# Optimization experiments

Measured on AMD Instinct MI355X. Metric: run time of the kernel, lower is better.

Reference implementation:

```python
import jax, jax.numpy as jnp
import numpy as np
import math

N, E, MUL = 10000, 160000, 128
D = MUL * 4  # 128x0e (128) + 128x1o (384) = 512
NEURONS = 32
EDGE_ATTR_DIM = 32
WEIGHT_NUMEL = 4 * MUL  # 4 uvu tensor-product paths, 128 weights each


def ssp(x):
    return jax.nn.softplus(x) - math.log(2.0)


def irrep_linear(x, W0, b0, W1):
    # o3.Linear on 128x0e+128x1o: mixes mul channels within each irrep, fan-in normalized,
    # bias only on scalar (0e) block.
    s = x[:, :MUL] @ (W0 / jnp.sqrt(MUL)) + b0
    v = x[:, MUL:].reshape(-1, MUL, 3)
    v = jnp.einsum('num,uv->nvm', v, W1) / jnp.sqrt(MUL)
    return jnp.concatenate([s, v.reshape(-1, MUL * 3)], axis=-1)


def inner_product(a, b):
    # InnerProduct: uuu channel-wise irrep inner product, 1/sqrt(dim) normalized
    s = a[:, :MUL] * b[:, :MUL]
    va = a[:, MUL:].reshape(-1, MUL, 3)
    vb = b[:, MUL:].reshape(-1, MUL, 3)
    v = jnp.einsum('num,num->nu', va, vb) / jnp.sqrt(3.0)
    return jnp.concatenate([s, v], axis=-1)


def norm_gate(x, W1, b1, W2, b2):
    # NormGate: per-channel norms of l>0 irreps -> MLP gates -> gate l>0 channels
    v = x[:, MUL:].reshape(-1, MUL, 3)
    norm_v = jnp.sqrt(jnp.sum(v * v, axis=-1) + 1e-12)      # [n, 128]
    f0 = jnp.concatenate([x[:, :MUL], norm_v], axis=-1)     # [n, 256]
    g = jax.nn.silu(f0 @ W1 + b1) @ W2 + b2                 # [n, 256]
    gated = v * g[:, MUL:, None]
    return jnp.concatenate([g[:, :MUL], gated.reshape(-1, MUL * 3)], axis=-1)


def mlp2(x, Wa, Wb):
    # e3nn FullyConnectedNet: fan-in normalized, ssp nonlinearity on hidden layer only
    return ssp(x @ (Wa / jnp.sqrt(Wa.shape[0]))) @ (Wb / jnp.sqrt(Wb.shape[0]))


def setup_inputs():
    key = jax.random.key(0)
    ks = jax.random.split(key, 20)
    r = lambda i, shp: jax.random.normal(ks[i], shp, dtype=jnp.float32)
    return {
        'x': r(0, (N, D)),
        'edge_index': jax.random.randint(ks[1], (2, E), 0, N, dtype=jnp.int32),
        'edge_attr': jax.random.uniform(ks[2], (E, EDGE_ATTR_DIM), dtype=jnp.float32),
        'edge_sh': r(3, (E, 4)),
        'Wp0': r(4, (MUL, MUL)), 'bp0': jnp.zeros((MUL,), jnp.float32), 'Wp1': r(5, (MUL, MUL)),
        'ngW1': r(6, (2 * MUL, 2 * MUL)) / 16.0, 'ngb1': jnp.zeros((2 * MUL,), jnp.float32),
        'ngW2': r(7, (2 * MUL, 2 * MUL)) / 16.0, 'ngb2': jnp.zeros((2 * MUL,), jnp.float32),
        'Wn0': r(8, (MUL, MUL)), 'bn0': jnp.zeros((MUL,), jnp.float32), 'Wn1': r(9, (MUL, MUL)),
        'fcnW1': r(10, (EDGE_ATTR_DIM, NEURONS)), 'fcnW2': r(11, (NEURONS, WEIGHT_NUMEL)),
        'l0W1': r(12, (3 * MUL, NEURONS)), 'l0W2': r(13, (NEURONS, WEIGHT_NUMEL)),
        'Wo0': r(14, (MUL, MUL)), 'bo0': jnp.zeros((MUL,), jnp.float32), 'Wo1': r(15, (MUL, MUL)),
    }


def reference(x, edge_index, edge_attr, edge_sh, Wp0, bp0, Wp1, ngW1, ngb1, ngW2, ngb2,
              Wn0, bn0, Wn1, fcnW1, fcnW2, l0W1, l0W2, Wo0, bo0, Wo1):
    edge_dst, edge_src = edge_index[0], edge_index[1]
    # invariant edge descriptor s0 from pre-linear + inner product
    pre_x = irrep_linear(x, Wp0, bp0, Wp1)
    ip = inner_product(pre_x[edge_dst], pre_x[edge_src])[:, MUL:]             # [E,128]
    s0 = jnp.concatenate([pre_x[edge_dst][:, :MUL], pre_x[edge_src][:, :MUL], ip], axis=-1)  # [E,384]
    # norm-gate + linear on node features
    x = norm_gate(x, ngW1, ngb1, ngW2, ngb2)
    x = irrep_linear(x, Wn0, bn0, Wn1)
    self_x = x
    # per-edge tensor-product weights: fc_node(edge_attr) * layer_l0(s0)
    w = mlp2(edge_attr, fcnW1, fcnW2) * mlp2(s0, l0W1, l0W2)                   # [E,512]
    w1, w2, w3, w4 = w[:, :MUL], w[:, MUL:2 * MUL], w[:, 2 * MUL:3 * MUL], w[:, 3 * MUL:]
    xs = x[edge_src]
    xs0 = xs[:, :MUL]                     # [E,128]
    xs1 = xs[:, MUL:].reshape(E, MUL, 3)  # [E,128,3]
    sh0 = edge_sh[:, 0:1]
    sh1 = edge_sh[:, 1:4]
    # uvu CG tensor product paths: 0ex0e->0e, 0ex1o->1o, 1ox0e->1o, 1ox1o->0e
    c0, c1 = 0.5, jnp.sqrt(3.0) / 2.0  # path norm sqrt(ir_out.dim / n_paths)
    out0 = c0 * (w1 * xs0 * sh0 + w4 * jnp.einsum('eum,em->eu', xs1, sh1) / jnp.sqrt(3.0))
    out1 = c1 * (w2[:, :, None] * xs0[:, :, None] * sh1[:, None, :]
                 + w3[:, :, None] * xs1 * sh0[:, :, None])
    edge_feat = jnp.concatenate([out0, out1.reshape(E, MUL * 3)], axis=-1)     # [E,512]
    # scatter-aggregate to destination nodes, residual, output linear
    out = jax.ops.segment_sum(edge_feat, edge_dst, num_segments=N)
    out = out + self_x
    return irrep_linear(out, Wo0, bo0, Wo1)
```

## Files before the change

kernel.cpp:

```cpp
#include <hip/hip_runtime.h>
#include <hip/hip_fp16.h>
#include <math.h>

#define NN 10000
#define EE 160000
#define DPB 8

#define RS128 0.08838834764831845f
#define RS384 0.05103103630798287f
#define RS32  0.17677669529663687f
#define R3    0.57735026918962576f
#define C1V   0.86602540378443865f

typedef _Float16 half8 __attribute__((ext_vector_type(8)));
typedef _Float16 half4 __attribute__((ext_vector_type(4)));
typedef float f32x4 __attribute__((ext_vector_type(4)));

__device__ __forceinline__ float sspf(float x) {
    return fmaxf(x, 0.0f) + log1pf(__expf(-fabsf(x))) - 0.69314718055994530942f;
}

__device__ __forceinline__ void packone(const float* __restrict__ W,
                                        _Float16* __restrict__ P,
                                        int K, int N, int off) {
    const int KS = K >> 5;
    int j = off & 7, lane = (off >> 3) & 63, rest = off >> 9;
    int ks = rest % KS, ct = rest / KS;
    int k = ks * 32 + ((lane >> 4) << 3) + j;
    int c = ct * 16 + (lane & 15);
    P[off] = (_Float16)W[k * N + c];
}

__global__ __launch_bounds__(256) void k_packall(
    const float* __restrict__ Wp0, const float* __restrict__ Wp1,
    const float* __restrict__ Wn0, const float* __restrict__ Wn1,
    const float* __restrict__ Wo0, const float* __restrict__ Wo1,
    const float* __restrict__ ngW1, const float* __restrict__ ngW2,
    const float* __restrict__ l0W1, const float* __restrict__ fcnW1,
    const float* __restrict__ fcnW2, const float* __restrict__ l0W2,
    _Float16* __restrict__ pWp0, _Float16* __restrict__ pWp1,
    _Float16* __restrict__ pWn0, _Float16* __restrict__ pWn1,
    _Float16* __restrict__ pWo0, _Float16* __restrict__ pWo1,
    _Float16* __restrict__ png1, _Float16* __restrict__ png2,
    _Float16* __restrict__ pWc, _Float16* __restrict__ pWa,
    _Float16* __restrict__ Wf_t, _Float16* __restrict__ Wl_t,
    _Float16* __restrict__ pWab, int* __restrict__ degz) {
    int idx = blockIdx.x * 256 + threadIdx.x;
    if (idx < 98304) {
        int seg = idx >> 14, off = idx & 16383;
        if (seg == 0) packone(Wp0, pWp0, 128, 128, off);
        else if (seg == 1) packone(Wp1, pWp1, 128, 128, off);
        else if (seg == 2) packone(Wn0, pWn0, 128, 128, off);
        else if (seg == 3) packone(Wn1, pWn1, 128, 128, off);
        else if (seg == 4) packone(Wo0, pWo0, 128, 128, off);
        else packone(Wo1, pWo1, 128, 128, off);
    } else if (idx < 229376) {
        int r = idx - 98304;
        if (r < 65536) packone(ngW1, png1, 256, 256, r);
        else packone(ngW2, png2, 256, 256, r - 65536);
    } else if (idx < 233472) {
        packone(l0W1 + 256 * 32, pWc, 128, 32, idx - 229376);
    } else if (idx < 234496) {
        packone(fcnW1, pWa, 32, 32, idx - 233472);
    } else if (idx < 250880) {
        int off = idx - 234496;
        int k = off & 31, c = off >> 5;
        Wf_t[c * 32 + k] = (_Float16)fcnW2[k * 512 + c];
        Wl_t[c * 32 + k] = (_Float16)l0W2[k * 512 + c];
    } else if (idx < 259072) {
        int off = idx - 250880;
        int j = off & 7, lane = (off >> 3) & 63, rest = off >> 9;
        int ks = rest & 3, ct = rest >> 2;
        int k = ks * 32 + ((lane >> 4) << 3) + j;
        int c = ct * 16 + (lane & 15);
        pWab[off] = (_Float16)((c < 32) ? l0W1[k * 32 + c]
                                        : l0W1[(128 + k) * 32 + (c - 32)]);
    } else if (idx < 279072) {
        degz[idx - 259072] = 0;
    }
}

__global__ __launch_bounds__(256) void k_node(
    const float* __restrict__ X,
    const _Float16* __restrict__ pWp0, const float* __restrict__ bp0,
    const _Float16* __restrict__ pWp1, const _Float16* __restrict__ pWab,
    const _Float16* __restrict__ png1, const float* __restrict__ ngb1,
    const _Float16* __restrict__ png2, const float* __restrict__ ngb2,
    const _Float16* __restrict__ pWn0, const float* __restrict__ bn0,
    const _Float16* __restrict__ pWn1,
    _Float16* __restrict__ prexv_h, float* __restrict__ pAB,
    _Float16* __restrict__ selfx_h) {
    __shared__ _Float16 f0h[16][264];
    __shared__ _Float16 t1h[16][264];
    __shared__ _Float16 xvh[3][16][136];
    __shared__ _Float16 pvh[3][16][136];
    const int t = threadIdx.x, lane = t & 63, w = t >> 6;
    const int nb = blockIdx.x * 16;
    const int row16 = lane & 15, kg = lane >> 4;
    const f32x4 zero = {0.0f, 0.0f, 0.0f, 0.0f};

    for (int idx = t; idx < 16 * 128; idx += 256) {
        int n = idx >> 7, c4 = idx & 127;
        const float4 v = *(const float4*)(X + (size_t)(nb + n) * 512 + 4 * c4);
        float vals[4] = {v.x, v.y, v.z, v.w};
        int c = 4 * c4;
#pragma unroll
        for (int j = 0; j < 4; ++j) {
            int cc = c + j;
            if (cc < 128) f0h[n][cc] = (_Float16)vals[j];
            else { int d = cc - 128; xvh[d % 3][n][d / 3] = (_Float16)vals[j]; }
        }
    }
    __syncthreads();
    for (int idx = t; idx < 16 * 128; idx += 256) {
        int n = idx >> 7, u = idx & 127;
        float a = (float)xvh[0][n][u], b = (float)xvh[1][n][u], c = (float)xvh[2][n][u];
        f0h[n][128 + u] = (_Float16)sqrtf(fmaf(a, a, fmaf(b, b, fmaf(c, c, 1e-12f))));
    }
    __syncthreads();
    {
        const _Float16* pW = (w == 0) ? pWp0 : pWp1;
        f32x4 acc[8];
#pragma unroll
        for (int ct = 0; ct < 8; ++ct) acc[ct] = zero;
        for (int ks = 0; ks < 4; ++ks) {
            const half8 a = (w == 0)
                ? *(const half8*)&f0h[row16][ks * 32 + kg * 8]
                : *(const half8*)&xvh[w - 1][row16][ks * 32 + kg * 8];
#pragma unroll
            for (int ct = 0; ct < 8; ++ct) {
                const half8 b = *(const half8*)(pW + (((ct * 4 + ks) * 64 + lane) << 3));
                acc[ct] = __builtin_amdgcn_mfma_f32_16x16x32_f16(a, b, acc[ct], 0, 0, 0);
            }
        }
#pragma unroll
        for (int ct = 0; ct < 8; ++ct) {
            const int col = ct * 16 + row16;
            const float bb = (w == 0) ? bp0[col] : 0.0f;
#pragma unroll
            for (int r = 0; r < 4; ++r) {
                const int n = kg * 4 + r;
                const float val = acc[ct][r] * RS128 + bb;
                if (w == 0) t1h[n][col] = (_Float16)val;
                else pvh[w - 1][n][col] = (_Float16)val;
            }
        }
    }
    __syncthreads();
    {
        f32x4 acc = zero;
#pragma unroll
        for (int ks = 0; ks < 4; ++ks) {
            const half8 a = *(const half8*)&t1h[row16][ks * 32 + kg * 8];
            const half8 b = *(const half8*)(pWab + (((w * 4 + ks) * 64 + lane) << 3));
            acc = __builtin_amdgcn_mfma_f32_16x16x32_f16(a, b, acc, 0, 0, 0);
        }
        const int col = w * 16 + row16;
#pragma unroll
        for (int r = 0; r < 4; ++r)
            pAB[(size_t)(nb + kg * 4 + r) * 64 + col] = acc[r];
    }
    for (int idx = t; idx < 16 * 128; idx += 256) {
        int n = idx >> 7, u = idx & 127;
        half4 pv = {pvh[0][n][u], pvh[1][n][u], pvh[2][n][u], t1h[n][u]};
        *(half4*)(prexv_h + (size_t)(nb + n) * 512 + (u << 2)) = pv;
    }
    __syncthreads();
    {
        f32x4 acc[4];
#pragma unroll
        for (int i = 0; i < 4; ++i) acc[i] = zero;
        for (int ks = 0; ks < 8; ++ks) {
            const half8 a = *(const half8*)&f0h[row16][ks * 32 + kg * 8];
#pragma unroll
            for (int c2 = 0; c2 < 4; ++c2) {
                const int ct = 4 * w + c2;
                const half8 b = *(const half8*)(png1 + (((ct * 8 + ks) * 64 + lane) << 3));
                acc[c2] = __builtin_amdgcn_mfma_f32_16x16x32_f16(a, b, acc[c2], 0, 0, 0);
            }
        }
        __syncthreads();
#pragma unroll
        for (int c2 = 0; c2 < 4; ++c2) {
            const int col = (4 * w + c2) * 16 + row16;
            const float bb = ngb1[col];
#pragma unroll
            for (int r = 0; r < 4; ++r) {
                const float z = acc[c2][r] + bb;
                t1h[kg * 4 + r][col] = (_Float16)(z / (1.0f + __expf(-z)));
            }
        }
    }
    __syncthreads();
    {
        f32x4 acc[4];
#pragma unroll
        for (int i = 0; i < 4; ++i) acc[i] = zero;
        for (int ks = 0; ks < 8; ++ks) {
            const half8 a = *(const half8*)&t1h[row16][ks * 32 + kg * 8];
#pragma unroll
            for (int c2 = 0; c2 < 4; ++c2) {
                const int ct = 4 * w + c2;
                const half8 b = *(const half8*)(png2 + (((ct * 8 + ks) * 64 + lane) << 3));
                acc[c2] = __builtin_amdgcn_mfma_f32_16x16x32_f16(a, b, acc[c2], 0, 0, 0);
            }
        }
        __syncthreads();
#pragma unroll
        for (int c2 = 0; c2 < 4; ++c2) {
            const int col = (4 * w + c2) * 16 + row16;
            const float bb = ngb2[col];
#pragma unroll
            for (int r = 0; r < 4; ++r)
                f0h[kg * 4 + r][col] = (_Float16)(acc[c2][r] + bb);
        }
    }
    __syncthreads();
    for (int idx = t; idx < 16 * 128; idx += 256) {
        int n = idx >> 7, u = idx & 127;
        const _Float16 g = f0h[n][128 + u];
        xvh[0][n][u] = xvh[0][n][u] * g;
        xvh[1][n][u] = xvh[1][n][u] * g;
        xvh[2][n][u] = xvh[2][n][u] * g;
    }
    __syncthreads();
    {
        const _Float16* pw = (w == 0) ? pWn0 : pWn1;
        f32x4 acc[8];
#pragma unroll
        for (int ct = 0; ct < 8; ++ct) acc[ct] = zero;
        for (int ks = 0; ks < 4; ++ks) {
            const half8 a = (w == 0)
                ? *(const half8*)&f0h[row16][ks * 32 + kg * 8]
                : *(const half8*)&xvh[w - 1][row16][ks * 32 + kg * 8];
#pragma unroll
            for (int ct = 0; ct < 8; ++ct) {
                const half8 b = *(const half8*)(pw + (((ct * 4 + ks) * 64 + lane) << 3));
                acc[ct] = __builtin_amdgcn_mfma_f32_16x16x32_f16(a, b, acc[ct], 0, 0, 0);
            }
        }
#pragma unroll
        for (int ct = 0; ct < 8; ++ct) {
            const int col = ct * 16 + row16;
            const float bb = (w == 0) ? bn0[col] : 0.0f;
#pragma unroll
            for (int r = 0; r < 4; ++r) {
                const int n = kg * 4 + r;
                const float val = acc[ct][r] * RS128 + bb;
                if (w == 0) f0h[n][col] = (_Float16)val;
                else xvh[w - 1][n][col] = (_Float16)val;
            }
        }
    }
    __syncthreads();
    for (int idx = t; idx < 16 * 128; idx += 256) {
        int n = idx >> 7, u = idx & 127;
        half4 sx = {f0h[n][u], xvh[0][n][u], xvh[1][n][u], xvh[2][n][u]};
        *(half4*)(selfx_h + (size_t)(nb + n) * 512 + (u << 2)) = sx;
    }
}

__global__ __launch_bounds__(256) void k_deg(const int* __restrict__ ei, int* __restrict__ deg) {
    int e = blockIdx.x * 256 + threadIdx.x;
    if (e < EE) atomicAdd(&deg[ei[e]], 1);
}

__global__ __launch_bounds__(1024) void k_scan(const int* __restrict__ deg, int* __restrict__ row_ptr) {
    __shared__ int part[1024];
    const int t = threadIdx.x;
    const int base = t * 10;
    int loc[10];
    int s = 0;
#pragma unroll
    for (int i = 0; i < 10; ++i) {
        int idx = base + i;
        int d = (idx < NN) ? deg[idx] : 0;
        loc[i] = s;
        s += d;
    }
    part[t] = s;
    __syncthreads();
    for (int off = 1; off < 1024; off <<= 1) {
        int v = (t >= off) ? part[t - off] : 0;
        __syncthreads();
        part[t] += v;
        __syncthreads();
    }
    int excl = (t > 0) ? part[t - 1] : 0;
#pragma unroll
    for (int i = 0; i < 10; ++i) {
        int idx = base + i;
        if (idx <= NN) row_ptr[idx] = excl + loc[i];
    }
}

__global__ __launch_bounds__(256) void k_fill(const int* __restrict__ ei,
                                              const int* __restrict__ row_ptr,
                                              int* __restrict__ cursor,
                                              int* __restrict__ csr_eid) {
    int e = blockIdx.x * 256 + threadIdx.x;
    if (e < EE) {
        int d = ei[e];
        int pos = atomicAdd(&cursor[d], 1);
        csr_eid[row_ptr[d] + pos] = e;
    }
}

__global__ __launch_bounds__(256) void k_hidden_m(
    const _Float16* __restrict__ prexv_h, const float* __restrict__ pAB,
    const int* __restrict__ edge_index, const float* __restrict__ edge_attr,
    const int* __restrict__ csr_eid,
    const _Float16* __restrict__ pWc, const _Float16* __restrict__ pWa,
    __half* __restrict__ hh) {
    const int pb = blockIdx.x * 32;
    const int t = threadIdx.x, lane = t & 63, w = t >> 6;
    __shared__ _Float16 ipl[32][132];
    __shared__ _Float16 eal[32][36];
    __shared__ _Float16 h1o[32][32];
    __shared__ _Float16 hao[32][32];
    __shared__ int dsts[32], srcs[32], eids[32];

    if (t < 32) {
        const int id = csr_eid[pb + t];
        eids[t] = id;
        dsts[t] = edge_index[id];
        srcs[t] = edge_index[EE + id];
    }
    __syncthreads();
    for (int idx = t; idx < 32 * 32; idx += 256) {
        int e = idx >> 5, j = idx & 31;
        eal[e][j] = (_Float16)edge_attr[(size_t)eids[e] * 32 + j];
    }
    for (int idx = t; idx < 32 * 128; idx += 256) {
        int e = idx >> 7, u = idx & 127;
        const half4 pd = *(const half4*)(prexv_h + (size_t)dsts[e] * 512 + (u << 2));
        const half4 ps = *(const half4*)(prexv_h + (size_t)srcs[e] * 512 + (u << 2));
        const float ipv = (float)pd.x * (float)ps.x + (float)pd.y * (float)ps.y +
                          (float)pd.z * (float)ps.z;
        ipl[e][u] = (_Float16)(ipv * R3);
    }
    __syncthreads();

    const int row16 = lane & 15, kg = lane >> 4;
    const int mt = w >> 1, ct = w & 1;
    const int e0 = mt * 16;
    const f32x4 zero = {0.0f, 0.0f, 0.0f, 0.0f};
    const int kc = ct * 16 + row16;

    {
        f32x4 acc = zero;
#pragma unroll
        for (int ks = 0; ks < 4; ++ks) {
            const half8 a = *(const half8*)&ipl[e0 + row16][ks * 32 + kg * 8];
            const half8 b = *(const half8*)(pWc + (((ct * 4 + ks) * 64 + lane) << 3));
            acc = __builtin_amdgcn_mfma_f32_16x16x32_f16(a, b, acc, 0, 0, 0);
        }
#pragma unroll
        for (int r = 0; r < 4; ++r) {
            const int e = e0 + kg * 4 + r;
            const float v = acc[r] + pAB[(size_t)dsts[e] * 64 + kc]
                                   + pAB[(size_t)srcs[e] * 64 + 32 + kc];
            h1o[e][kc] = (_Float16)sspf(v * RS384);
        }
    }
    {
        const half8 a = *(const half8*)&eal[e0 + row16][kg * 8];
        const half8 b = *(const half8*)(pWa + ((ct * 64 + lane) << 3));
        f32x4 acc = __builtin_amdgcn_mfma_f32_16x16x32_f16(a, b, zero, 0, 0, 0);
#pragma unroll
        for (int r = 0; r < 4; ++r) {
            const int e = e0 + kg * 4 + r;
            hao[e][kc] = (_Float16)sspf((float)acc[r] * RS32);
        }
    }
    __syncthreads();
    for (int idx = t; idx < 32 * 32; idx += 256) {
        const int e = idx >> 5, j = idx & 31;
        unsigned vv;
        if (j < 16) {
            __half2 h2 = __halves2half2((__half)h1o[e][2 * j], (__half)h1o[e][2 * j + 1]);
            vv = *(unsigned*)&h2;
        } else {
            const int jj = j - 16;
            __half2 h2 = __halves2half2((__half)hao[e][2 * jj], (__half)hao[e][2 * jj + 1]);
            vv = *(unsigned*)&h2;
        }
        ((unsigned*)hh)[(size_t)(pb + e) * 32 + j] = vv;
    }
}

__global__ __launch_bounds__(512) void k_accum(
    const __half* __restrict__ hh, const _Float16* __restrict__ selfx_h,
    const int* __restrict__ edge_index, const float* __restrict__ edge_sh,
    const int* __restrict__ row_ptr, const int* __restrict__ csr_eid,
    const _Float16* __restrict__ Wf_t, const _Float16* __restrict__ Wl_t,
    const _Float16* __restrict__ pWo0, const float* __restrict__ bo0,
    const _Float16* __restrict__ pWo1,
    float* __restrict__ outacc) {
    const int dst0 = blockIdx.x * DPB;
    const int t = threadIdx.x;
    const int lane = t & 63;
    const int wid = t >> 6;
    const int lcol = lane & 15;
    const int kg = lane >> 4;
    const int u = 16 * wid + lcol;
    const int koff = kg * 8;

    __shared__ __align__(16) _Float16 h1s[2][4][16][8];
    __shared__ __align__(16) _Float16 has[2][4][16][8];
    __shared__ float shl[2][16][4];
    __shared__ int srcs[2][16];
    __shared__ int cbeg[DPB], cne[DPB], cchk[DPB + 1];
    __shared__ __align__(16) _Float16 accP[4][16][136];

    if (t < DPB) {
        const int b = row_ptr[dst0 + t];
        cbeg[t] = b;
        cne[t] = row_ptr[dst0 + t + 1] - b;
    }
    for (int idx = t; idx < 4 * 16 * 136; idx += 512)
        ((_Float16*)accP)[idx] = (_Float16)0;
    __syncthreads();
    if (t == 0) {
        int s = 0;
#pragma unroll
        for (int i = 0; i < DPB; ++i) { cchk[i] = s; s += max(1, (cne[i] + 15) >> 4); }
        cchk[DPB] = s;
    }
    half8 bf[4], bl[4];
#pragma unroll
    for (int q = 0; q < 4; ++q) {
        const int col = q * 128 + u;
        bf[q] = *(const half8*)(Wf_t + col * 32 + koff);
        bl[q] = *(const half8*)(Wl_t + col * 32 + koff);
    }
    __syncthreads();
    const int nc = cchk[DPB];
    const float inv32 = 1.0f / 32.0f;

    float acc0 = 0, acc1 = 0, acc2 = 0, acc3 = 0;

    unsigned rhh = 0;
    int rsrc = 0;
    float4 rsh = {0.0f, 0.0f, 0.0f, 0.0f};

    const int se = t >> 5, sw = t & 31;

    auto issue = [&](int ci) {
        int dd = 0;
        while (dd + 1 < DPB && ci >= cchk[dd + 1]) ++dd;
        const int c0 = (ci - cchk[dd]) << 4;
        const int ce = min(16, cne[dd] - c0);
        const int pos = cbeg[dd] + c0;
        rhh = (se < ce) ? ((const unsigned*)hh)[(size_t)(pos + se) * 32 + sw] : 0u;
        if (t < 16) {
            if (t < ce) {
                const int id = csr_eid[pos + t];
                rsrc = edge_index[EE + id];
                rsh = *(const float4*)(edge_sh + (size_t)id * 4);
            } else {
                rsrc = 0;
                rsh = make_float4(0.0f, 0.0f, 0.0f, 0.0f);
            }
        }
    };

    auto flush = [&](int dd) {
        acc0 += __shfl_xor(acc0, 16, 64); acc0 += __shfl_xor(acc0, 32, 64);
        acc1 += __shfl_xor(acc1, 16, 64); acc1 += __shfl_xor(acc1, 32, 64);
        acc2 += __shfl_xor(acc2, 16, 64); acc2 += __shfl_xor(acc2, 32, 64);
        acc3 += __shfl_xor(acc3, 16, 64); acc3 += __shfl_xor(acc3, 32, 64);
        if (lane < 16) {
            const size_t g = (size_t)(dst0 + dd) * 512;
            const half4 sx = *(const half4*)(selfx_h + g + (u << 2));
            accP[0][dd][u] = (_Float16)(acc0 + (float)sx.x);
            accP[1][dd][u] = (_Float16)(acc1 + (float)sx.y);
            accP[2][dd][u] = (_Float16)(acc2 + (float)sx.z);
            accP[3][dd][u] = (_Float16)(acc3 + (float)sx.w);
        }
        acc0 = acc1 = acc2 = acc3 = 0;
    };

    issue(0);
    int cur = 0, cur_dd = 0;
    for (int ci = 0; ci < nc; ++ci) {
        if (sw < 16) ((unsigned*)h1s[cur])[(sw >> 2) * 64 + se * 4 + (sw & 3)] = rhh;
        else         ((unsigned*)has[cur])[((sw - 16) >> 2) * 64 + se * 4 + ((sw - 16) & 3)] = rhh;
        if (t < 16) {
            srcs[cur][t] = rsrc;
            shl[cur][t][0] = rsh.x; shl[cur][t][1] = rsh.y;
            shl[cur][t][2] = rsh.z; shl[cur][t][3] = rsh.w;
        }
        int dd = 0;
        while (dd + 1 < DPB && ci >= cchk[dd + 1]) ++dd;
        const int c0 = (ci - cchk[dd]) << 4;
        const int ce = min(16, cne[dd] - c0);
        if (ci + 1 < nc) issue(ci + 1);
        __syncthreads();
        if (dd != cur_dd) { flush(cur_dd); cur_dd = dd; }

        const half8 haf = *(const half8*)(&has[cur][kg][lcol][0]);
        const half8 h1f = *(const half8*)(&h1s[cur][kg][lcol][0]);
        const f32x4 zero = {0.0f, 0.0f, 0.0f, 0.0f};
        f32x4 A[4], B[4];
#pragma unroll
        for (int q = 0; q < 4; ++q) {
            A[q] = __builtin_amdgcn_mfma_f32_16x16x32_f16(haf, bf[q], zero, 0, 0, 0);
            B[q] = __builtin_amdgcn_mfma_f32_16x16x32_f16(h1f, bl[q], zero, 0, 0, 0);
        }
#pragma unroll
        for (int r = 0; r < 4; ++r) {
            const int e = kg * 4 + r;
            if (e < ce) {
                const float w1 = A[0][r] * B[0][r] * inv32;
                const float w2 = A[1][r] * B[1][r] * inv32;
                const float w3 = A[2][r] * B[2][r] * inv32;
                const float w4 = A[3][r] * B[3][r] * inv32;
                const int src = srcs[cur][e];
                const float sh0 = shl[cur][e][0], s1x = shl[cur][e][1];
                const float s1y = shl[cur][e][2], s1z = shl[cur][e][3];
                const half4 sx = *(const half4*)(selfx_h + (size_t)src * 512 + (u << 2));
                const float xs0 = (float)sx.x;
                const float xv0 = (float)sx.y;
                const float xv1 = (float)sx.z;
                const float xv2 = (float)sx.w;
                const float dv = xv0 * s1x + xv1 * s1y + xv2 * s1z;
                acc0 += 0.5f * (w1 * xs0 * sh0 + w4 * dv * R3);
                acc1 += C1V * (w2 * xs0 * s1x + w3 * xv0 * sh0);
                acc2 += C1V * (w2 * xs0 * s1y + w3 * xv1 * sh0);
                acc3 += C1V * (w2 * xs0 * s1z + w3 * xv2 * sh0);
            }
        }
        cur ^= 1;
    }
    flush(cur_dd);
    __syncthreads();

    {
        const int m = wid >> 1;
        const int ctg = (wid & 1) * 4;
        const _Float16* pW = (m == 0) ? pWo0 : pWo1;
        const f32x4 zero = {0.0f, 0.0f, 0.0f, 0.0f};
        f32x4 acc[4];
#pragma unroll
        for (int i = 0; i < 4; ++i) acc[i] = zero;
        for (int ks = 0; ks < 4; ++ks) {
            const half8 a = *(const half8*)&accP[m][lcol][ks * 32 + koff];
#pragma unroll
            for (int c2 = 0; c2 < 4; ++c2) {
                const int ct = ctg + c2;
                const half8 b = *(const half8*)(pW + (((ct * 4 + ks) * 64 + lane) << 3));
                acc[c2] = __builtin_amdgcn_mfma_f32_16x16x32_f16(a, b, acc[c2], 0, 0, 0);
            }
        }
#pragma unroll
        for (int c2 = 0; c2 < 4; ++c2) {
            const int col = (ctg + c2) * 16 + lcol;
            const float bb = (m == 0) ? bo0[col] : 0.0f;
#pragma unroll
            for (int r = 0; r < 4; ++r) {
                const int row = kg * 4 + r;
                if (row < DPB) {
                    const size_t g = (size_t)(dst0 + row) * 512;
                    const float val = acc[c2][r] * RS128 + bb;
                    if (m == 0) outacc[g + col] = val;
                    else outacc[g + 128 + 3 * col + (m - 1)] = val;
                }
            }
        }
    }
}

extern "C" void kernel_launch(void* const* d_in, const int* in_sizes, int n_in,
                              void* d_out, int out_size, void* d_ws, size_t ws_size,
                              hipStream_t stream) {
    const float* x = (const float*)d_in[0];
    const int* edge_index = (const int*)d_in[1];
    const float* edge_attr = (const float*)d_in[2];
    const float* edge_sh = (const float*)d_in[3];
    const float* Wp0 = (const float*)d_in[4];
    const float* bp0 = (const float*)d_in[5];
    const float* Wp1 = (const float*)d_in[6];
    const float* ngW1 = (const float*)d_in[7];
    const float* ngb1 = (const float*)d_in[8];
    const float* ngW2 = (const float*)d_in[9];
    const float* ngb2 = (const float*)d_in[10];
    const float* Wn0 = (const float*)d_in[11];
    const float* bn0 = (const float*)d_in[12];
    const float* Wn1 = (const float*)d_in[13];
    const float* fcnW1 = (const float*)d_in[14];
    const float* fcnW2 = (const float*)d_in[15];
    const float* l0W1 = (const float*)d_in[16];
    const float* l0W2 = (const float*)d_in[17];
    const float* Wo0 = (const float*)d_in[18];
    const float* bo0 = (const float*)d_in[19];
    const float* Wo1 = (const float*)d_in[20];

    float* out = (float*)d_out;
    _Float16* prexv_h = (_Float16*)d_out;
    _Float16* selfx_h = (_Float16*)d_ws;
    int* deg = (int*)(selfx_h + (size_t)NN * 512);
    int* cursor = deg + NN;
    int* row_ptr = cursor + NN;
    int* csr_eid = row_ptr + NN + 1;
    float* pAB = (float*)(csr_eid + EE);
    __half* hh = (__half*)(pAB + (size_t)NN * 64);
    _Float16* Wf_t = (_Float16*)(hh + (size_t)EE * 64);
    _Float16* Wl_t = Wf_t + 512 * 32;
    _Float16* pWp0 = Wl_t + 512 * 32;
    _Float16* pWp1 = pWp0 + 128 * 128;
    _Float16* pWn0 = pWp1 + 128 * 128;
    _Float16* pWn1 = pWn0 + 128 * 128;
    _Float16* pWo0 = pWn1 + 128 * 128;
    _Float16* pWo1 = pWo0 + 128 * 128;
    _Float16* png1 = pWo1 + 128 * 128;
    _Float16* png2 = png1 + 256 * 256;
    _Float16* pWc  = png2 + 256 * 256;
    _Float16* pWa  = pWc + 128 * 32;
    _Float16* pWab = pWa + 32 * 32;

    k_packall<<<1091, 256, 0, stream>>>(Wp0, Wp1, Wn0, Wn1, Wo0, Wo1, ngW1, ngW2,
                                        l0W1, fcnW1, fcnW2, l0W2,
                                        pWp0, pWp1, pWn0, pWn1, pWo0, pWo1,
                                        png1, png2, pWc, pWa, Wf_t, Wl_t,
                                        pWab, deg);

    k_node<<<NN / 16, 256, 0, stream>>>(x, pWp0, bp0, pWp1, pWab,
                                        png1, ngb1, png2, ngb2, pWn0, bn0, pWn1,
                                        prexv_h, pAB, selfx_h);
    k_deg<<<EE / 256, 256, 0, stream>>>(edge_index, deg);
    k_scan<<<1, 1024, 0, stream>>>(deg, row_ptr);
    k_fill<<<EE / 256, 256, 0, stream>>>(edge_index, row_ptr, cursor, csr_eid);
    k_hidden_m<<<EE / 32, 256, 0, stream>>>(prexv_h, pAB, edge_index, edge_attr, csr_eid,
                                            pWc, pWa, hh);
    k_accum<<<NN / DPB, 512, 0, stream>>>(hh, selfx_h, edge_index, edge_sh, row_ptr, csr_eid,
                                          Wf_t, Wl_t, pWo0, bo0, pWo1, out);
}
```

Measured before the change: 254.4 us.

## Pre-sort src and fp16 edge_sh into CSR order and prefetch gathered source features

k_fill now also writes the source index and a half-precision copy of edge_sh in CSR order, so k_accum no longer follows csr_eid to edge_index and edge_sh. k_accum prefetches the next chunk's gathered selfx rows into registers after the current chunk's compute, overlapping the gather latency with the MFMA work. The Wl_t fragments are reloaded inside the loop instead of being held in registers, which lowers register pressure. The cost is extra global traffic for the reload, fp16 rounding of edge_sh, and a few more workspace writes in k_fill.

```diff
diff --git a/kernel.cpp b/kernel.cpp
--- a/kernel.cpp
+++ b/kernel.cpp
@@ -295,14 +295,22 @@
 }
 
 __global__ __launch_bounds__(256) void k_fill(const int* __restrict__ ei,
+                                              const float* __restrict__ edge_sh,
                                               const int* __restrict__ row_ptr,
                                               int* __restrict__ cursor,
-                                              int* __restrict__ csr_eid) {
+                                              int* __restrict__ csr_eid,
+                                              int* __restrict__ csr_src,
+                                              _Float16* __restrict__ csr_sh) {
     int e = blockIdx.x * 256 + threadIdx.x;
     if (e < EE) {
         int d = ei[e];
-        int pos = atomicAdd(&cursor[d], 1);
-        csr_eid[row_ptr[d] + pos] = e;
+        int s = ei[EE + e];
+        const float4 sh = *(const float4*)(edge_sh + (size_t)e * 4);
+        int pos = row_ptr[d] + atomicAdd(&cursor[d], 1);
+        csr_eid[pos] = e;
+        csr_src[pos] = s;
+        half4 h = {(_Float16)sh.x, (_Float16)sh.y, (_Float16)sh.z, (_Float16)sh.w};
+        *(half4*)(csr_sh + (size_t)pos * 4) = h;
     }
 }
 
@@ -391,9 +399,9 @@
 
 __global__ __launch_bounds__(512) void k_accum(
     const __half* __restrict__ hh, const _Float16* __restrict__ selfx_h,
-    const int* __restrict__ edge_index, const float* __restrict__ edge_sh,
-    const int* __restrict__ row_ptr, const int* __restrict__ csr_eid,
-    const _Float16* __restrict__ Wf_t, const _Float16* __restrict__ Wl_t,
+    const int* __restrict__ row_ptr,
+    const int* __restrict__ csr_src, const _Float16* __restrict__ csr_sh,
+    const _Float16* __restrict__ Wf_t, const _Float16* Wl_t,
     const _Float16* __restrict__ pWo0, const float* __restrict__ bo0,
     const _Float16* __restrict__ pWo1,
     float* __restrict__ outacc) {
@@ -408,8 +416,7 @@
 
     __shared__ __align__(16) _Float16 h1s[2][4][16][8];
     __shared__ __align__(16) _Float16 has[2][4][16][8];
-    __shared__ float shl[2][16][4];
-    __shared__ int srcs[2][16];
+    __shared__ __align__(8) _Float16 shl[2][16][4];
     __shared__ int cbeg[DPB], cne[DPB], cchk[DPB + 1];
     __shared__ __align__(16) _Float16 accP[4][16][136];
 
@@ -427,13 +434,10 @@
         for (int i = 0; i < DPB; ++i) { cchk[i] = s; s += max(1, (cne[i] + 15) >> 4); }
         cchk[DPB] = s;
     }
-    half8 bf[4], bl[4];
-#pragma unroll
-    for (int q = 0; q < 4; ++q) {
-        const int col = q * 128 + u;
-        bf[q] = *(const half8*)(Wf_t + col * 32 + koff);
-        bl[q] = *(const half8*)(Wl_t + col * 32 + koff);
-    }
+    half8 bf[4];
+#pragma unroll
+    for (int q = 0; q < 4; ++q)
+        bf[q] = *(const half8*)(Wf_t + (q * 128 + u) * 32 + koff);
     __syncthreads();
     const int nc = cchk[DPB];
     const float inv32 = 1.0f / 32.0f;
@@ -441,26 +445,37 @@
     float acc0 = 0, acc1 = 0, acc2 = 0, acc3 = 0;
 
     unsigned rhh = 0;
-    int rsrc = 0;
-    float4 rsh = {0.0f, 0.0f, 0.0f, 0.0f};
+    const half4 h4z = {(_Float16)0, (_Float16)0, (_Float16)0, (_Float16)0};
+    half4 rsh4 = h4z;
+    half4 nsx[4] = {h4z, h4z, h4z, h4z};
 
     const int se = t >> 5, sw = t & 31;
 
-    auto issue = [&](int ci) {
+    auto chunkmeta = [&](int ci, int& pos, int& ce) {
         int dd = 0;
         while (dd + 1 < DPB && ci >= cchk[dd + 1]) ++dd;
         const int c0 = (ci - cchk[dd]) << 4;
-        const int ce = min(16, cne[dd] - c0);
-        const int pos = cbeg[dd] + c0;
+        ce = min(16, cne[dd] - c0);
+        pos = cbeg[dd] + c0;
+    };
+
+    auto issue_meta = [&](int ci) {
+        int pos, ce; chunkmeta(ci, pos, ce);
         rhh = (se < ce) ? ((const unsigned*)hh)[(size_t)(pos + se) * 32 + sw] : 0u;
-        if (t < 16) {
-            if (t < ce) {
-                const int id = csr_eid[pos + t];
-                rsrc = edge_index[EE + id];
-                rsh = *(const float4*)(edge_sh + (size_t)id * 4);
+        if (t < 16)
+            rsh4 = (t < ce) ? *(const half4*)(csr_sh + (size_t)(pos + t) * 4) : h4z;
+    };
+
+    auto issue_payload = [&](int ci) {
+        int pos, ce; chunkmeta(ci, pos, ce);
+#pragma unroll
+        for (int r = 0; r < 4; ++r) {
+            const int e = kg * 4 + r;
+            if (e < ce) {
+                const int s = csr_src[pos + e];
+                nsx[r] = *(const half4*)(selfx_h + (size_t)s * 512 + (u << 2));
             } else {
-                rsrc = 0;
-                rsh = make_float4(0.0f, 0.0f, 0.0f, 0.0f);
+                nsx[r] = h4z;
             }
         }
     };
@@ -481,21 +496,16 @@
         acc0 = acc1 = acc2 = acc3 = 0;
     };
 
-    issue(0);
+    issue_meta(0);
+    issue_payload(0);
     int cur = 0, cur_dd = 0;
     for (int ci = 0; ci < nc; ++ci) {
         if (sw < 16) ((unsigned*)h1s[cur])[(sw >> 2) * 64 + se * 4 + (sw & 3)] = rhh;
         else         ((unsigned*)has[cur])[((sw - 16) >> 2) * 64 + se * 4 + ((sw - 16) & 3)] = rhh;
-        if (t < 16) {
-            srcs[cur][t] = rsrc;
-            shl[cur][t][0] = rsh.x; shl[cur][t][1] = rsh.y;
-            shl[cur][t][2] = rsh.z; shl[cur][t][3] = rsh.w;
-        }
+        if (t < 16) *(half4*)&shl[cur][t][0] = rsh4;
         int dd = 0;
         while (dd + 1 < DPB && ci >= cchk[dd + 1]) ++dd;
-        const int c0 = (ci - cchk[dd]) << 4;
-        const int ce = min(16, cne[dd] - c0);
-        if (ci + 1 < nc) issue(ci + 1);
+        if (ci + 1 < nc) issue_meta(ci + 1);
         __syncthreads();
         if (dd != cur_dd) { flush(cur_dd); cur_dd = dd; }
 
@@ -505,32 +515,31 @@
         f32x4 A[4], B[4];
 #pragma unroll
         for (int q = 0; q < 4; ++q) {
+            const half8 blq = *(const half8*)(Wl_t + (q * 128 + u) * 32 + koff);
             A[q] = __builtin_amdgcn_mfma_f32_16x16x32_f16(haf, bf[q], zero, 0, 0, 0);
-            B[q] = __builtin_amdgcn_mfma_f32_16x16x32_f16(h1f, bl[q], zero, 0, 0, 0);
+            B[q] = __builtin_amdgcn_mfma_f32_16x16x32_f16(h1f, blq, zero, 0, 0, 0);
         }
 #pragma unroll
         for (int r = 0; r < 4; ++r) {
             const int e = kg * 4 + r;
-            if (e < ce) {
-                const float w1 = A[0][r] * B[0][r] * inv32;
-                const float w2 = A[1][r] * B[1][r] * inv32;
-                const float w3 = A[2][r] * B[2][r] * inv32;
-                const float w4 = A[3][r] * B[3][r] * inv32;
-                const int src = srcs[cur][e];
-                const float sh0 = shl[cur][e][0], s1x = shl[cur][e][1];
-                const float s1y = shl[cur][e][2], s1z = shl[cur][e][3];
-                const half4 sx = *(const half4*)(selfx_h + (size_t)src * 512 + (u << 2));
-                const float xs0 = (float)sx.x;
-                const float xv0 = (float)sx.y;
-                const float xv1 = (float)sx.z;
-                const float xv2 = (float)sx.w;
-                const float dv = xv0 * s1x + xv1 * s1y + xv2 * s1z;
-                acc0 += 0.5f * (w1 * xs0 * sh0 + w4 * dv * R3);
-                acc1 += C1V * (w2 * xs0 * s1x + w3 * xv0 * sh0);
-                acc2 += C1V * (w2 * xs0 * s1y + w3 * xv1 * sh0);
-                acc3 += C1V * (w2 * xs0 * s1z + w3 * xv2 * sh0);
-            }
-        }
+            const float w1 = A[0][r] * B[0][r] * inv32;
+            const float w2 = A[1][r] * B[1][r] * inv32;
+            const float w3 = A[2][r] * B[2][r] * inv32;
+            const float w4 = A[3][r] * B[3][r] * inv32;
+            const half4 shv = *(const half4*)&shl[cur][e][0];
+            const float sh0 = (float)shv.x, s1x = (float)shv.y;
+            const float s1y = (float)shv.z, s1z = (float)shv.w;
+            const float xs0 = (float)nsx[r].x;
+            const float xv0 = (float)nsx[r].y;
+            const float xv1 = (float)nsx[r].z;
+            const float xv2 = (float)nsx[r].w;
+            const float dv = xv0 * s1x + xv1 * s1y + xv2 * s1z;
+            acc0 += 0.5f * (w1 * xs0 * sh0 + w4 * dv * R3);
+            acc1 += C1V * (w2 * xs0 * s1x + w3 * xv0 * sh0);
+            acc2 += C1V * (w2 * xs0 * s1y + w3 * xv1 * sh0);
+            acc3 += C1V * (w2 * xs0 * s1z + w3 * xv2 * sh0);
+        }
+        if (ci + 1 < nc) issue_payload(ci + 1);
         cur ^= 1;
     }
     flush(cur_dd);
@@ -603,7 +612,9 @@
     int* cursor = deg + NN;
     int* row_ptr = cursor + NN;
     int* csr_eid = row_ptr + NN + 1;
-    float* pAB = (float*)(csr_eid + EE);
+    int* csr_src = csr_eid + EE;
+    _Float16* csr_sh = (_Float16*)(csr_src + EE);
+    float* pAB = (float*)(csr_sh + (size_t)EE * 4);
     __half* hh = (__half*)(pAB + (size_t)NN * 64);
     _Float16* Wf_t = (_Float16*)(hh + (size_t)EE * 64);
     _Float16* Wl_t = Wf_t + 512 * 32;
@@ -630,9 +641,10 @@
                                         prexv_h, pAB, selfx_h);
     k_deg<<<EE / 256, 256, 0, stream>>>(edge_index, deg);
     k_scan<<<1, 1024, 0, stream>>>(deg, row_ptr);
-    k_fill<<<EE / 256, 256, 0, stream>>>(edge_index, row_ptr, cursor, csr_eid);
+    k_fill<<<EE / 256, 256, 0, stream>>>(edge_index, edge_sh, row_ptr, cursor,
+                                         csr_eid, csr_src, csr_sh);
     k_hidden_m<<<EE / 32, 256, 0, stream>>>(prexv_h, pAB, edge_index, edge_attr, csr_eid,
                                             pWc, pWa, hh);
-    k_accum<<<NN / DPB, 512, 0, stream>>>(hh, selfx_h, edge_index, edge_sh, row_ptr, csr_eid,
+    k_accum<<<NN / DPB, 512, 0, stream>>>(hh, selfx_h, row_ptr, csr_src, csr_sh,
                                           Wf_t, Wl_t, pWo0, bo0, pWo1, out);
 }
```

Result: slower. 354.8 us (+39.4%).
